# Performance work log

Hardware: AMD Instinct MI355X
Metric: run time of the kernel (lower is better)

Reference implementation:

```python
import jax, jax.numpy as jnp
import numpy as np
import math

HIDDEN = 256
D = 256  # attention_head_size (num_heads=1)
LN_EPS = 1e-5


def setup_inputs() -> dict:
    key = jax.random.key(0)
    ks = jax.random.split(key, 12)
    b, n = 8, 256
    s = 0.02
    return {
        "hidden_states": jax.random.normal(ks[0], (b, n, HIDDEN), jnp.float32),
        "structure_matrix": jax.random.normal(ks[1], (b, n, n, D), jnp.float32),
        "Wq": jax.random.normal(ks[2], (HIDDEN, D), jnp.float32) * s,
        "bq": jnp.zeros((D,), jnp.float32),
        "Wk": jax.random.normal(ks[3], (D, D), jnp.float32) * s,
        "bk": jnp.zeros((D,), jnp.float32),
        "Wv": jax.random.normal(ks[4], (HIDDEN, D), jnp.float32) * s,
        "bv": jnp.zeros((D,), jnp.float32),
        "Wo": jax.random.normal(ks[5], (D, D), jnp.float32) * s,
        "bo": jnp.zeros((D,), jnp.float32),
        "ln_gamma": jnp.ones((D,), jnp.float32),
        "ln_beta": jnp.zeros((D,), jnp.float32),
    }


def _layer_norm(x, gamma, beta):
    mu = jnp.mean(x, axis=-1, keepdims=True)
    var = jnp.mean(jnp.square(x - mu), axis=-1, keepdims=True)
    return (x - mu) * jax.lax.rsqrt(var + LN_EPS) * gamma + beta


def reference(hidden_states, structure_matrix, Wq, bq, Wk, bk, Wv, bv, Wo, bo, ln_gamma, ln_beta):
    # projections
    q = hidden_states @ Wq + bq            # [b, n, d]
    k = structure_matrix @ Wk + bk         # [b, l, r, d]
    v = hidden_states @ Wv + bv            # [b, n, d]
    # pair-biased attention: each (l, r) pair attends over all n tokens
    scores = jnp.einsum('bnd,blrd->blrn', q, k) / math.sqrt(D)  # [b, l, r, n]
    probs = jax.nn.softmax(scores, axis=-1)  # dropout is identity in eval
    ctx = jnp.einsum('blrn,bnd->blrd', probs, v)  # [b, l, r, d]
    out = ctx @ Wo + bo
    return _layer_norm(out + structure_matrix, ln_gamma, ln_beta)
```

## Files before the change

kernel.cpp:

```cpp
#include <hip/hip_runtime.h>
#include <hip/hip_bf16.h>

typedef __attribute__((ext_vector_type(8))) short short8v;
typedef __attribute__((ext_vector_type(4))) float f32x4;
typedef __attribute__((ext_vector_type(8))) unsigned short us8;
typedef const __attribute__((address_space(1))) void* gas_t;
typedef __attribute__((address_space(3))) void* las_t;

#define LDA 264

__device__ __forceinline__ unsigned short f2bf(float f) {
  union { __hip_bfloat16 h; unsigned short u; } c;
  c.h = __float2bfloat16(f);
  return c.u;
}
__device__ __forceinline__ unsigned int f2bf2(float lo, float hi) {
  union { __hip_bfloat162 h; unsigned int u; } c;
  c.h = __float22bfloat162_rn(make_float2(lo, hi));
  return c.u;
}

__global__ __launch_bounds__(256) void tr_wk(const float* __restrict__ Wk,
                                             float* __restrict__ WkT) {
  __shared__ float sT[64][65];
  const int b = blockIdx.x;
  const int bi = b >> 2, bj = b & 3;
  const int tid = threadIdx.x;
  const int r4 = tid >> 6, c64 = tid & 63;
#pragma unroll
  for (int p = 0; p < 16; p++)
    sT[c64][p * 4 + r4] = Wk[(bi * 64 + p * 4 + r4) * 256 + bj * 64 + c64];
  __syncthreads();
#pragma unroll
  for (int p = 0; p < 16; p++)
    WkT[(bj * 64 + p * 4 + r4) * 256 + bi * 64 + c64] = sT[p * 4 + r4][c64];
}

__global__ __launch_bounds__(256) void make_w(
    const float* __restrict__ WkT, const float* __restrict__ Wq,
    const float* __restrict__ Wv, const float* __restrict__ Wo,
    const float* __restrict__ bq, const float* __restrict__ bk,
    const float* __restrict__ bv, float* __restrict__ WA,
    float* __restrict__ WB, float* __restrict__ wb2,
    float* __restrict__ cq, float* __restrict__ cv, float* __restrict__ cb) {
  __shared__ float wq[256], wv[256], bqs[256], bvs[256];
  const int i = blockIdx.x, t = threadIdx.x;
  wq[t] = Wq[i * 256 + t];
  wv[t] = Wv[i * 256 + t];
  bqs[t] = bq[t];
  bvs[t] = bv[t];
  __syncthreads();
  float sa = 0.f, sb = 0.f;
#pragma unroll 8
  for (int d = 0; d < 256; d++) {
    sa = fmaf(wq[d], WkT[d * 256 + t], sa);
    sb = fmaf(wv[d], Wo[d * 256 + t], sb);
  }
  WA[i * 256 + t] = sa * 0.0625f;
  WB[i * 256 + t] = sb;
  if (t == 0) {
    float s = 0.f;
#pragma unroll 8
    for (int d = 0; d < 256; d++) s = fmaf(wq[d], bk[d], s);
    wb2[i] = s * 0.0625f;
  }
  if (i == 0) {
    float s1 = 0.f, s2 = 0.f;
#pragma unroll 8
    for (int d = 0; d < 256; d++) {
      s1 = fmaf(bqs[d], WkT[d * 256 + t], s1);
      s2 = fmaf(bvs[d], Wo[d * 256 + t], s2);
    }
    cq[t] = s1 * 0.0625f;
    cv[t] = s2;
    if (t == 0) {
      float s = 0.f;
      for (int d = 0; d < 256; d++) s = fmaf(bk[d], bqs[d], s);
      cb[0] = s * 0.0625f;
    }
  }
}

__global__ __launch_bounds__(256) void prep2(
    const float* __restrict__ hs, const float* __restrict__ WA,
    const float* __restrict__ WB, const float* __restrict__ wb2,
    const float* __restrict__ cq, const float* __restrict__ cv,
    const float* __restrict__ cb, unsigned short* __restrict__ W2c,
    unsigned short* __restrict__ V2c, float* __restrict__ bn) {
  __shared__ float rows[8][256];
  __shared__ float w2s[256];
  const int tid = threadIdx.x;
  const int g0 = blockIdx.x * 8;
#pragma unroll
  for (int j = 0; j < 8; j++) rows[j][tid] = hs[(size_t)(g0 + j) * 256 + tid];
  w2s[tid] = wb2[tid];
  __syncthreads();
  const float cqv = cq[tid], cvv = cv[tid];
  float aq[8], av[8];
#pragma unroll
  for (int j = 0; j < 8; j++) { aq[j] = cqv; av[j] = cvv; }
#pragma unroll 8
  for (int i = 0; i < 256; i++) {
    const float wa = WA[i * 256 + tid];
    const float wb = WB[i * 256 + tid];
#pragma unroll
    for (int j = 0; j < 8; j++) {
      aq[j] = fmaf(rows[j][i], wa, aq[j]);
      av[j] = fmaf(rows[j][i], wb, av[j]);
    }
  }
  const int bb = g0 >> 8, n0 = g0 & 255;
  {
    const int kc = tid >> 5, lhi = (tid >> 3) & 3, j = tid & 7;
    const int w = n0 >> 6, nt = (n0 >> 4) & 3, l0 = n0 & 15;
    unsigned short* dst = W2c + bb * 65536 + kc * 8192 + w * 2048 + nt * 512 +
                          lhi * 128 + l0 * 8 + j;
#pragma unroll
    for (int jj = 0; jj < 8; jj++) dst[jj * 8] = f2bf(aq[jj]);
  }
  {
    const int kc = n0 >> 5, lhi = (n0 >> 3) & 3;
    const int w = tid >> 6, nt = (tid >> 4) & 3, l16 = tid & 15;
    us8 vp;
#pragma unroll
    for (int j = 0; j < 8; j++) vp[j] = f2bf(av[j]);
    *(us8*)(V2c + bb * 65536 + kc * 8192 + w * 2048 + nt * 512 + lhi * 128 +
            l16 * 8) = vp;
  }
  if (tid < 8) {
    float s = 0.f;
    for (int i = 0; i < 256; i++) s = fmaf(rows[tid][i], w2s[i], s);
    bn[bb * 256 + n0 + tid] = s + cb[0];
  }
}

__device__ __forceinline__ void stage_b(const unsigned short* src_wave,
                                        unsigned short* lds_wave, int lane) {
#pragma unroll
  for (int i = 0; i < 4; i++) {
    const unsigned short* g = src_wave + i * 512 + lane * 8;
    unsigned short* l = lds_wave + i * 512;
    __builtin_amdgcn_global_load_lds((gas_t)g, (las_t)l, 16, 0, 0);
  }
}

__global__ __launch_bounds__(256, 2) void pair_attn10(
    const float* __restrict__ S, const float* __restrict__ bo,
    const float* __restrict__ gamma, const float* __restrict__ beta,
    const float* __restrict__ bn, const unsigned short* __restrict__ W2c,
    const unsigned short* __restrict__ V2c, float* __restrict__ out) {
  __shared__ unsigned short sA[64 * LDA];
  __shared__ unsigned short sB[2][8192];
  __shared__ float sRed[64 * 8];

  const int tid = threadIdx.x;
  const int w = tid >> 6;
  const int lane = tid & 63;
  const int l16 = lane & 15;
  const int lhi = lane >> 4;
  const int bid = blockIdx.x;
  const int idx = (bid & 7) * 1024 + (bid >> 3);
  const int rblk = idx & 3;
  const int lrow = (idx >> 2) & 255;
  const int bat = idx >> 10;

  const size_t base = ((size_t)((bat * 256 + lrow) * 256 + rblk * 64)) * 256;
  const float* Sblk = S + base;

#pragma unroll
  for (int it = 0; it < 8; it++) {
    const int c = tid + it * 256;
    const int row = c >> 5, col = (c & 31) << 3;
    const float4 u = *(const float4*)(Sblk + row * 256 + col);
    const float4 v = *(const float4*)(Sblk + row * 256 + col + 4);
    us8 p;
    unsigned int* pu = (unsigned int*)&p;
    pu[0] = f2bf2(u.x, u.y);
    pu[1] = f2bf2(u.z, u.w);
    pu[2] = f2bf2(v.x, v.y);
    pu[3] = f2bf2(v.z, v.w);
    *(us8*)(sA + row * LDA + col) = p;
  }
  float bnv[4];
#pragma unroll
  for (int nt = 0; nt < 4; nt++)
    bnv[nt] = bn[bat * 256 + w * 64 + nt * 16 + l16];
  __syncthreads();

  const unsigned short* W2b = W2c + (size_t)bat * 65536;
  const unsigned short* V2b = V2c + (size_t)bat * 65536;

  asm volatile("s_waitcnt vmcnt(0)" ::: "memory");
  __builtin_amdgcn_sched_barrier(0);

  stage_b(W2b + 0 * 8192 + w * 2048, &sB[0][w * 2048], lane);
  stage_b(W2b + 1 * 8192 + w * 2048, &sB[1][w * 2048], lane);

  f32x4 acc[4][4];
#pragma unroll
  for (int rt = 0; rt < 4; rt++)
#pragma unroll
    for (int nt = 0; nt < 4; nt++) acc[rt][nt] = (f32x4){0.f, 0.f, 0.f, 0.f};

#pragma unroll
  for (int q = 0; q < 8; q++) {
    asm volatile("s_waitcnt vmcnt(4)" ::: "memory");
    __builtin_amdgcn_sched_barrier(0);
    const unsigned short* bb = &sB[q & 1][w * 2048];
    short8v a[4], bf[4];
#pragma unroll
    for (int rt = 0; rt < 4; rt++)
      a[rt] = *(const short8v*)(sA + (rt * 16 + l16) * LDA + q * 32 + lhi * 8);
#pragma unroll
    for (int nt = 0; nt < 4; nt++)
      bf[nt] = *(const short8v*)(bb + nt * 512 + lane * 8);
    asm volatile("s_waitcnt lgkmcnt(0)" ::: "memory");
    __builtin_amdgcn_sched_barrier(0);
    if (q < 6)
      stage_b(W2b + (q + 2) * 8192 + w * 2048, &sB[q & 1][w * 2048], lane);
    else
      stage_b(V2b + (q - 6) * 8192 + w * 2048, &sB[q & 1][w * 2048], lane);
    __builtin_amdgcn_sched_barrier(0);
#pragma unroll
    for (int rt = 0; rt < 4; rt++)
#pragma unroll
      for (int nt = 0; nt < 4; nt++)
        acc[rt][nt] = __builtin_amdgcn_mfma_f32_16x16x32_bf16(
            a[rt], bf[nt], acc[rt][nt], 0, 0, 0);
  }

  asm volatile("s_waitcnt lgkmcnt(0)" ::: "memory");
  __builtin_amdgcn_s_barrier();
#pragma unroll
  for (int rt = 0; rt < 4; rt++)
#pragma unroll
    for (int nt = 0; nt < 4; nt++)
#pragma unroll
      for (int rg = 0; rg < 4; rg++)
        sA[(rt * 16 + lhi * 4 + rg) * LDA + (w * 64 + nt * 16 + l16)] =
            f2bf(__expf(acc[rt][nt][rg] + bnv[nt]));
  asm volatile("s_waitcnt lgkmcnt(0)" ::: "memory");
  __builtin_amdgcn_s_barrier();

  short8v onesv;
#pragma unroll
  for (int j = 0; j < 8; j++) onesv[j] = (short)0x3F80;
  f32x4 ps[4];
#pragma unroll
  for (int rt = 0; rt < 4; rt++) {
    ps[rt] = (f32x4){0.f, 0.f, 0.f, 0.f};
#pragma unroll
    for (int nt = 0; nt < 4; nt++) acc[rt][nt] = (f32x4){0.f, 0.f, 0.f, 0.f};
  }
#pragma unroll
  for (int q = 0; q < 8; q++) {
    if (q < 7) {
      asm volatile("s_waitcnt vmcnt(4)" ::: "memory");
    } else {
      asm volatile("s_waitcnt vmcnt(0)" ::: "memory");
    }
    __builtin_amdgcn_sched_barrier(0);
    const unsigned short* bb = &sB[q & 1][w * 2048];
    short8v a[4], bf[4];
#pragma unroll
    for (int rt = 0; rt < 4; rt++)
      a[rt] = *(const short8v*)(sA + (rt * 16 + l16) * LDA + q * 32 + lhi * 8);
#pragma unroll
    for (int nt = 0; nt < 4; nt++)
      bf[nt] = *(const short8v*)(bb + nt * 512 + lane * 8);
    asm volatile("s_waitcnt lgkmcnt(0)" ::: "memory");
    __builtin_amdgcn_sched_barrier(0);
    if (q < 6)
      stage_b(V2b + (q + 2) * 8192 + w * 2048, &sB[q & 1][w * 2048], lane);
    __builtin_amdgcn_sched_barrier(0);
#pragma unroll
    for (int rt = 0; rt < 4; rt++) {
#pragma unroll
      for (int nt = 0; nt < 4; nt++)
        acc[rt][nt] = __builtin_amdgcn_mfma_f32_16x16x32_bf16(
            a[rt], bf[nt], acc[rt][nt], 0, 0, 0);
      ps[rt] = __builtin_amdgcn_mfma_f32_16x16x32_bf16(a[rt], onesv, ps[rt],
                                                       0, 0, 0);
    }
  }
  __builtin_amdgcn_sched_barrier(0);

  float bov[4], gv[4], bev[4];
#pragma unroll
  for (int nt = 0; nt < 4; nt++) {
    const int col = w * 64 + nt * 16 + l16;
    bov[nt] = bo[col];
    gv[nt] = gamma[col];
    bev[nt] = beta[col];
  }
#pragma unroll
  for (int rt = 0; rt < 4; rt++)
#pragma unroll
    for (int rg = 0; rg < 4; rg++) {
      const int row = rt * 16 + lhi * 4 + rg;
      const float invr = 1.f / ps[rt][rg];
      const float* Srow = Sblk + row * 256;
      float s1 = 0.f, s2 = 0.f;
#pragma unroll
      for (int nt = 0; nt < 4; nt++) {
        const int col = w * 64 + nt * 16 + l16;
        const float val = acc[rt][nt][rg] * invr + bov[nt] + Srow[col];
        acc[rt][nt][rg] = val;
        s1 += val;
        s2 = fmaf(val, val, s2);
      }
      s1 += __shfl_xor(s1, 1); s2 += __shfl_xor(s2, 1);
      s1 += __shfl_xor(s1, 2); s2 += __shfl_xor(s2, 2);
      s1 += __shfl_xor(s1, 4); s2 += __shfl_xor(s2, 4);
      s1 += __shfl_xor(s1, 8); s2 += __shfl_xor(s2, 8);
      if (l16 == 0) { sRed[row * 8 + w] = s1; sRed[row * 8 + 4 + w] = s2; }
    }
  __syncthreads();

  float* O = out + base;
#pragma unroll
  for (int rt = 0; rt < 4; rt++)
#pragma unroll
    for (int rg = 0; rg < 4; rg++) {
      const int row = rt * 16 + lhi * 4 + rg;
      f32x4 sa = *(f32x4*)(sRed + row * 8);
      f32x4 sq = *(f32x4*)(sRed + row * 8 + 4);
      const float mean = (sa[0] + sa[1] + sa[2] + sa[3]) * (1.f / 256.f);
      const float ex2 = (sq[0] + sq[1] + sq[2] + sq[3]) * (1.f / 256.f);
      const float rstd = rsqrtf(ex2 - mean * mean + 1e-5f);
      float* Orow = O + row * 256;
#pragma unroll
      for (int nt = 0; nt < 4; nt++) {
        const int col = w * 64 + nt * 16 + l16;
        Orow[col] = (acc[rt][nt][rg] - mean) * rstd * gv[nt] + bev[nt];
      }
    }
}

extern "C" void kernel_launch(void* const* d_in, const int* in_sizes, int n_in,
                              void* d_out, int out_size, void* d_ws, size_t ws_size,
                              hipStream_t stream) {
  const float* hs    = (const float*)d_in[0];
  const float* S     = (const float*)d_in[1];
  const float* Wq    = (const float*)d_in[2];
  const float* bq    = (const float*)d_in[3];
  const float* Wk    = (const float*)d_in[4];
  const float* bk    = (const float*)d_in[5];
  const float* Wv    = (const float*)d_in[6];
  const float* bv    = (const float*)d_in[7];
  const float* Wo    = (const float*)d_in[8];
  const float* bo    = (const float*)d_in[9];
  const float* gamma = (const float*)d_in[10];
  const float* beta  = (const float*)d_in[11];

  unsigned short* W2c = (unsigned short*)d_ws;
  unsigned short* V2c = W2c + 8 * 256 * 256;
  float* WA  = (float*)(V2c + 8 * 256 * 256);
  float* WB  = WA + 256 * 256;
  float* WkT = WB + 256 * 256;
  float* wb2 = WkT + 256 * 256;
  float* cq  = wb2 + 256;
  float* cv  = cq + 256;
  float* cb  = cv + 256;
  float* bnp = cb + 256;

  tr_wk<<<16, 256, 0, stream>>>(Wk, WkT);
  make_w<<<256, 256, 0, stream>>>(WkT, Wq, Wv, Wo, bq, bk, bv, WA, WB, wb2,
                                  cq, cv, cb);
  prep2<<<256, 256, 0, stream>>>(hs, WA, WB, wb2, cq, cv, cb, W2c, V2c, bnp);
  pair_attn10<<<8192, 256, 0, stream>>>(S, bo, gamma, beta, bnp, W2c, V2c,
                                        (float*)d_out);
}
```

Measured before the change: 501.5 us.

## Load B operands directly from global into registers, drop LDS double buffer

Removes the double-buffered LDS staging of the W2/V2 operand tiles via global_load_lds and instead has each wave load its B fragments straight from global memory (L2-resident) into registers for every MFMA step. This frees 32 KB of LDS per block, and the launch-bounds hint is raised from 2 to 3 blocks per CU for higher occupancy. The trade-off is losing the explicit prefetch pipeline and the manual wait/sched barriers: global load latency now sits directly in front of each MFMA batch and has to be hidden by more resident waves.

```diff
diff --git a/kernel.cpp b/kernel.cpp
--- a/kernel.cpp
+++ b/kernel.cpp
@@ -4,8 +4,6 @@
 typedef __attribute__((ext_vector_type(8))) short short8v;
 typedef __attribute__((ext_vector_type(4))) float f32x4;
 typedef __attribute__((ext_vector_type(8))) unsigned short us8;
-typedef const __attribute__((address_space(1))) void* gas_t;
-typedef __attribute__((address_space(3))) void* las_t;
 
 #define LDA 264
 
@@ -134,23 +132,12 @@
   }
 }
 
-__device__ __forceinline__ void stage_b(const unsigned short* src_wave,
-                                        unsigned short* lds_wave, int lane) {
-#pragma unroll
-  for (int i = 0; i < 4; i++) {
-    const unsigned short* g = src_wave + i * 512 + lane * 8;
-    unsigned short* l = lds_wave + i * 512;
-    __builtin_amdgcn_global_load_lds((gas_t)g, (las_t)l, 16, 0, 0);
-  }
-}
-
-__global__ __launch_bounds__(256, 2) void pair_attn10(
+__global__ __launch_bounds__(256, 3) void pair_attn16(
     const float* __restrict__ S, const float* __restrict__ bo,
     const float* __restrict__ gamma, const float* __restrict__ beta,
     const float* __restrict__ bn, const unsigned short* __restrict__ W2c,
     const unsigned short* __restrict__ V2c, float* __restrict__ out) {
   __shared__ unsigned short sA[64 * LDA];
-  __shared__ unsigned short sB[2][8192];
   __shared__ float sRed[64 * 8];
 
   const int tid = threadIdx.x;
@@ -187,14 +174,8 @@
     bnv[nt] = bn[bat * 256 + w * 64 + nt * 16 + l16];
   __syncthreads();
 
-  const unsigned short* W2b = W2c + (size_t)bat * 65536;
-  const unsigned short* V2b = V2c + (size_t)bat * 65536;
-
-  asm volatile("s_waitcnt vmcnt(0)" ::: "memory");
-  __builtin_amdgcn_sched_barrier(0);
-
-  stage_b(W2b + 0 * 8192 + w * 2048, &sB[0][w * 2048], lane);
-  stage_b(W2b + 1 * 8192 + w * 2048, &sB[1][w * 2048], lane);
+  const unsigned short* Wb = W2c + (size_t)bat * 65536 + w * 2048;
+  const unsigned short* Vb = V2c + (size_t)bat * 65536 + w * 2048;
 
   f32x4 acc[4][4];
 #pragma unroll
@@ -204,23 +185,13 @@
 
 #pragma unroll
   for (int q = 0; q < 8; q++) {
-    asm volatile("s_waitcnt vmcnt(4)" ::: "memory");
-    __builtin_amdgcn_sched_barrier(0);
-    const unsigned short* bb = &sB[q & 1][w * 2048];
     short8v a[4], bf[4];
+#pragma unroll
+    for (int nt = 0; nt < 4; nt++)
+      bf[nt] = *(const short8v*)(Wb + q * 8192 + nt * 512 + lane * 8);
 #pragma unroll
     for (int rt = 0; rt < 4; rt++)
       a[rt] = *(const short8v*)(sA + (rt * 16 + l16) * LDA + q * 32 + lhi * 8);
-#pragma unroll
-    for (int nt = 0; nt < 4; nt++)
-      bf[nt] = *(const short8v*)(bb + nt * 512 + lane * 8);
-    asm volatile("s_waitcnt lgkmcnt(0)" ::: "memory");
-    __builtin_amdgcn_sched_barrier(0);
-    if (q < 6)
-      stage_b(W2b + (q + 2) * 8192 + w * 2048, &sB[q & 1][w * 2048], lane);
-    else
-      stage_b(V2b + (q - 6) * 8192 + w * 2048, &sB[q & 1][w * 2048], lane);
-    __builtin_amdgcn_sched_barrier(0);
 #pragma unroll
     for (int rt = 0; rt < 4; rt++)
 #pragma unroll
@@ -228,9 +199,8 @@
         acc[rt][nt] = __builtin_amdgcn_mfma_f32_16x16x32_bf16(
             a[rt], bf[nt], acc[rt][nt], 0, 0, 0);
   }
-
-  asm volatile("s_waitcnt lgkmcnt(0)" ::: "memory");
-  __builtin_amdgcn_s_barrier();
+  __syncthreads();
+
 #pragma unroll
   for (int rt = 0; rt < 4; rt++)
 #pragma unroll
@@ -239,8 +209,7 @@
       for (int rg = 0; rg < 4; rg++)
         sA[(rt * 16 + lhi * 4 + rg) * LDA + (w * 64 + nt * 16 + l16)] =
             f2bf(__expf(acc[rt][nt][rg] + bnv[nt]));
-  asm volatile("s_waitcnt lgkmcnt(0)" ::: "memory");
-  __builtin_amdgcn_s_barrier();
+  __syncthreads();
 
   short8v onesv;
 #pragma unroll
@@ -254,25 +223,13 @@
   }
 #pragma unroll
   for (int q = 0; q < 8; q++) {
-    if (q < 7) {
-      asm volatile("s_waitcnt vmcnt(4)" ::: "memory");
-    } else {
-      asm volatile("s_waitcnt vmcnt(0)" ::: "memory");
-    }
-    __builtin_amdgcn_sched_barrier(0);
-    const unsigned short* bb = &sB[q & 1][w * 2048];
     short8v a[4], bf[4];
+#pragma unroll
+    for (int nt = 0; nt < 4; nt++)
+      bf[nt] = *(const short8v*)(Vb + q * 8192 + nt * 512 + lane * 8);
 #pragma unroll
     for (int rt = 0; rt < 4; rt++)
       a[rt] = *(const short8v*)(sA + (rt * 16 + l16) * LDA + q * 32 + lhi * 8);
-#pragma unroll
-    for (int nt = 0; nt < 4; nt++)
-      bf[nt] = *(const short8v*)(bb + nt * 512 + lane * 8);
-    asm volatile("s_waitcnt lgkmcnt(0)" ::: "memory");
-    __builtin_amdgcn_sched_barrier(0);
-    if (q < 6)
-      stage_b(V2b + (q + 2) * 8192 + w * 2048, &sB[q & 1][w * 2048], lane);
-    __builtin_amdgcn_sched_barrier(0);
 #pragma unroll
     for (int rt = 0; rt < 4; rt++) {
 #pragma unroll
@@ -283,7 +240,6 @@
                                                        0, 0, 0);
     }
   }
-  __builtin_amdgcn_sched_barrier(0);
 
   float bov[4], gv[4], bev[4];
 #pragma unroll
@@ -368,6 +324,6 @@
   make_w<<<256, 256, 0, stream>>>(WkT, Wq, Wv, Wo, bq, bk, bv, WA, WB, wb2,
                                   cq, cv, cb);
   prep2<<<256, 256, 0, stream>>>(hs, WA, WB, wb2, cq, cv, cb, W2c, V2c, bnp);
-  pair_attn10<<<8192, 256, 0, stream>>>(S, bo, gamma, beta, bnp, W2c, V2c,
+  pair_attn16<<<8192, 256, 0, stream>>>(S, bo, gamma, beta, bnp, W2c, V2c,
                                         (float*)d_out);
 }
```

Result: faster. 483.9 us (-3.5%).
